# Kernel optimization log

Measured on AMD Instinct MI355X. Metric: run time of the kernel, lower is better.

Reference implementation:

```python
import jax, jax.numpy as jnp
import numpy as np

D = 768          # hidden_size
N_HEADS = 12
HEAD_DIM = D // N_HEADS  # 64
WINDOW = 128 // 2        # local_attention // 2 = 64 tokens each side
ROPE_THETA = 10000.0     # local_rope_theta


def _rope_freqs(T, dtype=jnp.float32):
    # complex rotation factors e^{i * pos * inv_freq}, shape [T, HEAD_DIM//2]
    inv_freq = 1.0 / (ROPE_THETA ** (jnp.arange(0, HEAD_DIM, 2, dtype=dtype) / HEAD_DIM))
    ang = jnp.arange(T, dtype=dtype)[:, None] * inv_freq[None, :]
    return jnp.exp(1j * ang.astype(jnp.complex64))


def _apply_rope(x, freqs):
    # x: [B, T, N, H]; split into (2, H//2) pairs as in the source reshape
    B, T, N, H = x.shape
    pairs = x.reshape(B, T, N, 2, H // 2)
    c = pairs[..., 0, :] + 1j * pairs[..., 1, :]          # [B,T,N,H//2]
    rot = c * freqs[None, :, None, :]                      # broadcast over B, heads
    out = jnp.stack([jnp.real(rot), jnp.imag(rot)], axis=-1)  # [B,T,N,H//2,2]
    return out.reshape(B, T, N, H)  # attention_scaling = 1.0 for default rope


def setup_inputs() -> dict:
    key = jax.random.key(0)
    k1, k2, k3 = jax.random.split(key, 3)
    B, T = 4, 2048
    hidden_states = jax.random.normal(k1, (B, T, D), dtype=jnp.float32)
    attention_mask = jnp.ones((B, T), dtype=jnp.int32)
    Wqkv = jax.random.normal(k2, (3 * D, D), dtype=jnp.float32) * (1.0 / np.sqrt(D))
    Wo = jax.random.normal(k3, (D, D), dtype=jnp.float32) * (1.0 / np.sqrt(D))
    return {"hidden_states": hidden_states, "attention_mask": attention_mask,
            "Wqkv": Wqkv, "Wo": Wo}


def reference(hidden_states, attention_mask, Wqkv, Wo):
    B, T, _ = hidden_states.shape
    # fused QKV projection (no bias in ModernBERT)
    qkv = jnp.einsum('btd,ed->bte', hidden_states, Wqkv)   # [B,T,3D]
    q, k, v = jnp.split(qkv, 3, axis=-1)
    to_heads = lambda x: x.reshape(B, T, N_HEADS, HEAD_DIM)
    q, k, v = to_heads(q), to_heads(k), to_heads(v)
    # rotary embedding (complex multiply)
    freqs = _rope_freqs(T)
    q = _apply_rope(q, freqs)
    k = _apply_rope(k, freqs)
    # sliding-window + padding mask
    pos = jnp.arange(T)
    window = jnp.abs(pos[:, None] - pos[None, :]) <= WINDOW   # [T,T]
    pad = attention_mask.astype(jnp.bool_)                    # [B,T]
    allowed = window[None, None, :, :] & pad[:, None, :, None] & pad[:, None, None, :]
    # eager SDPA
    scale = 1.0 / np.sqrt(HEAD_DIM)
    scores = jnp.einsum('bqnh,bknh->bnqk', q, k) * scale      # [B,N,T,T]
    scores = jnp.where(allowed, scores, jnp.finfo(scores.dtype).min)
    probs = jax.nn.softmax(scores, axis=-1)
    attn = jnp.einsum('bnqk,bknh->bqnh', probs, v)            # [B,T,N,H]
    attn = attn.reshape(B, T, D)
    return jnp.einsum('btd,ed->bte', attn, Wo)                # output proj
```

## Files before the change

### kernel.cpp

```cpp
#include <hip/hip_runtime.h>
#include <hip/hip_bf16.h>
#include <math.h>

#define BATCH 4
#define SEQ   2048
#define DMODEL 768
#define NHEADS 12
#define HDIM  64
#define WIN   64
#define QKV_LD 2304

typedef __attribute__((ext_vector_type(8))) short bf16x8;
typedef __attribute__((ext_vector_type(4))) float f32x4;

typedef __attribute__((address_space(1))) const unsigned int guint;
typedef __attribute__((address_space(3))) unsigned int luint;

__device__ inline void gl_lds16(const __hip_bfloat16* g, __hip_bfloat16* l) {
    __builtin_amdgcn_global_load_lds((guint*)g, (luint*)l, 16, 0, 0);
}

__device__ inline void to_out(float* p, float v) { *p = v; }
__device__ inline void to_out(__hip_bfloat16* p, float v) { *p = __float2bfloat16(v); }

#define N4_HID  (BATCH * SEQ * DMODEL / 4)
#define N4_WQKV (QKV_LD * DMODEL / 4)
#define N4_WO   (DMODEL * DMODEL / 4)
#define N_ROPE  (SEQ * 32)
#define SETUP_TOTAL (N4_HID + N4_WQKV + N4_WO + N_ROPE)

__device__ inline void cast4(const float* in, __hip_bfloat16* out, int i) {
    float4 v = ((const float4*)in)[i];
    union { ushort4 u; __hip_bfloat16 h[4]; } o;
    o.h[0] = __float2bfloat16(v.x); o.h[1] = __float2bfloat16(v.y);
    o.h[2] = __float2bfloat16(v.z); o.h[3] = __float2bfloat16(v.w);
    ((ushort4*)out)[i] = o.u;
}

__global__ __launch_bounds__(256) void setup_kernel(const float* __restrict__ hidden,
                                                    const float* __restrict__ Wqkv,
                                                    const float* __restrict__ Wo,
                                                    __hip_bfloat16* __restrict__ hid_bf,
                                                    __hip_bfloat16* __restrict__ wqkv_bf,
                                                    __hip_bfloat16* __restrict__ wo_bf,
                                                    float2* __restrict__ tab) {
    int id = blockIdx.x * 256 + threadIdx.x;
    if (id < N4_HID) {
        cast4(hidden, hid_bf, id);
    } else if (id < N4_HID + N4_WQKV) {
        cast4(Wqkv, wqkv_bf, id - N4_HID);
    } else if (id < N4_HID + N4_WQKV + N4_WO) {
        cast4(Wo, wo_bf, id - N4_HID - N4_WQKV);
    } else if (id < SETUP_TOTAL) {
        int idx = id - (N4_HID + N4_WQKV + N4_WO);
        int t = idx >> 5, j = idx & 31;
        const float L2T_OVER_32 = 13.287712379549449f / 32.0f;
        float inv = exp2f(-(float)j * L2T_OVER_32);
        float s, c;
        sincosf((float)t * inv, &s, &c);
        tab[idx] = make_float2(c, s);
    }
}

template <typename OutT>
__global__ __launch_bounds__(256) void gemm_nt_bf16(const __hip_bfloat16* __restrict__ A,
                                                    const __hip_bfloat16* __restrict__ B,
                                                    OutT* __restrict__ C,
                                                    int lda, int ldb, int ldc, int K,
                                                    const float2* __restrict__ rope_tab) {
    __shared__ __align__(16) char smem[32768];
    __hip_bfloat16* As = (__hip_bfloat16*)smem;
    __hip_bfloat16* Bs = (__hip_bfloat16*)(smem + 16384);

    const int tid  = threadIdx.x;
    const int lane = tid & 63;
    const int wave = tid >> 6;
    const int wr   = wave >> 1;
    const int wc   = wave & 1;
    const int fr   = lane & 15;
    const int quad = lane >> 4;

    const int bid = blockIdx.x;
    const int x   = bid & 7;
    const int j   = bid >> 3;
    const int m0  = (x * 8 + (j & 7)) * 128;
    const int n0  = (j >> 3) * 128;

    f32x4 acc[4][4];
#pragma unroll
    for (int i = 0; i < 4; i++)
#pragma unroll
        for (int jj = 0; jj < 4; jj++) acc[i][jj] = (f32x4){0.f, 0.f, 0.f, 0.f};

    for (int k0 = 0; k0 < K; k0 += 64) {
        __syncthreads();
#pragma unroll
        for (int c = 0; c < 4; c++) {
            int t = (wave * 4 + c) * 64 + lane;
            int row = t >> 3, ch = t & 7;
            int gcol = (ch ^ (row & 7)) * 8;
            gl_lds16(A + (size_t)(m0 + row) * lda + k0 + gcol, As + t * 8);
            gl_lds16(B + (size_t)(n0 + row) * ldb + k0 + gcol, Bs + t * 8);
        }
        __syncthreads();

#pragma unroll
        for (int ks = 0; ks < 2; ks++) {
            bf16x8 af[4], bf_[4];
#pragma unroll
            for (int mi = 0; mi < 4; mi++) {
                int row = wr * 64 + mi * 16 + fr;
                int pos = (ks * 4 + quad) ^ (row & 7);
                af[mi] = *(const bf16x8*)(As + row * 64 + pos * 8);
            }
#pragma unroll
            for (int ni = 0; ni < 4; ni++) {
                int row = wc * 64 + ni * 16 + fr;
                int pos = (ks * 4 + quad) ^ (row & 7);
                bf_[ni] = *(const bf16x8*)(Bs + row * 64 + pos * 8);
            }
#pragma unroll
            for (int mi = 0; mi < 4; mi++)
#pragma unroll
                for (int ni = 0; ni < 4; ni++)
                    acc[mi][ni] = __builtin_amdgcn_mfma_f32_16x16x32_bf16(af[mi], bf_[ni], acc[mi][ni], 0, 0, 0);
        }
    }

    const int b0 = n0 + wc * 64;
    if (rope_tab != nullptr && b0 < 2 * DMODEL) {
#pragma unroll
        for (int mi = 0; mi < 4; mi++) {
#pragma unroll
            for (int r = 0; r < 4; r++) {
                int t = (m0 + wr * 64 + mi * 16 + quad * 4 + r) & (SEQ - 1);
#pragma unroll
                for (int ni = 0; ni < 2; ni++) {
                    float2 cs = rope_tab[t * 32 + ni * 16 + fr];
                    float x0 = acc[mi][ni][r], x1 = acc[mi][ni + 2][r];
                    acc[mi][ni][r]     = x0 * cs.x - x1 * cs.y;
                    acc[mi][ni + 2][r] = x0 * cs.y + x1 * cs.x;
                }
            }
        }
    }

    __syncthreads();
    OutT* patch = (OutT*)smem + wave * (16 * 72);
    constexpr int NV = sizeof(OutT);

#pragma unroll
    for (int mi = 0; mi < 4; mi++) {
#pragma unroll
        for (int ni = 0; ni < 4; ni++)
#pragma unroll
            for (int r = 0; r < 4; r++)
                to_out(&patch[(quad * 4 + r) * 72 + ni * 16 + fr], acc[mi][ni][r]);
        __syncthreads();
        {
            int prow = lane >> 2, seg = lane & 3;
            const uint4* src = (const uint4*)(patch + prow * 72 + seg * 16);
            OutT* dst = &C[(size_t)(m0 + wr * 64 + mi * 16 + prow) * ldc + b0 + seg * 16];
#pragma unroll
            for (int v = 0; v < NV; v++)
                ((uint4*)dst)[v] = src[v];
        }
        __syncthreads();
    }
}

#define PLD  192

__global__ __launch_bounds__(256) void attn_kernel(const __hip_bfloat16* __restrict__ qkv,
                                                   const int* __restrict__ mask,
                                                   __hip_bfloat16* __restrict__ attn) {
    __shared__ __align__(16) char smem[49152];
    __hip_bfloat16* Ks = (__hip_bfloat16*)smem;
    __hip_bfloat16* Pb = (__hip_bfloat16*)smem;
    __hip_bfloat16* Vt = (__hip_bfloat16*)(smem + 24576);

    const int tid  = threadIdx.x;
    const int lane = tid & 63;
    const int wave = tid >> 6;
    const int fr   = lane & 15;
    const int quad = lane >> 4;

    const int bid  = blockIdx.x;
    const int x    = bid & 7;
    const int j    = bid >> 3;
    const int b    = x >> 1;
    const int q0   = ((x & 1) * 16 + (j & 15)) * 64;
    const int head = j >> 4;

    const int klo = max(0, q0 - WIN);
    const int khi = min(SEQ, q0 + 64 + WIN);
    const int nk  = khi - klo;
    const int nt  = nk >> 4;
    const int nkc = nk >> 5;

    const size_t rowbase = (size_t)(b * SEQ) * QKV_LD + head * HDIM;

    for (int task = tid; task < nk * 8; task += 256) {
        int row = task >> 3, g = task & 7;
        uint4 v = *(const uint4*)(qkv + rowbase + (size_t)(klo + row) * QKV_LD + DMODEL + g * 8);
        *(uint4*)(Ks + row * 64 + (g ^ (row & 7)) * 8) = v;
    }
    {
        int h = lane;
        const __hip_bfloat16* vb = qkv + rowbase + 2 * DMODEL + h;
        int ng = nk >> 3;
        for (int g = wave; g < ng; g += 4) {
            unsigned int u0, u1, u2, u3;
            {
                unsigned short a0 = *(const unsigned short*)(vb + (size_t)(klo + g * 8 + 0) * QKV_LD);
                unsigned short a1 = *(const unsigned short*)(vb + (size_t)(klo + g * 8 + 1) * QKV_LD);
                unsigned short a2 = *(const unsigned short*)(vb + (size_t)(klo + g * 8 + 2) * QKV_LD);
                unsigned short a3 = *(const unsigned short*)(vb + (size_t)(klo + g * 8 + 3) * QKV_LD);
                unsigned short a4 = *(const unsigned short*)(vb + (size_t)(klo + g * 8 + 4) * QKV_LD);
                unsigned short a5 = *(const unsigned short*)(vb + (size_t)(klo + g * 8 + 5) * QKV_LD);
                unsigned short a6 = *(const unsigned short*)(vb + (size_t)(klo + g * 8 + 6) * QKV_LD);
                unsigned short a7 = *(const unsigned short*)(vb + (size_t)(klo + g * 8 + 7) * QKV_LD);
                u0 = (unsigned int)a0 | ((unsigned int)a1 << 16);
                u1 = (unsigned int)a2 | ((unsigned int)a3 << 16);
                u2 = (unsigned int)a4 | ((unsigned int)a5 << 16);
                u3 = (unsigned int)a6 | ((unsigned int)a7 << 16);
            }
            int cs = g ^ (h & 7);
            *(uint4*)(Vt + h * PLD + cs * 8) = make_uint4(u0, u1, u2, u3);
        }
    }

    const int qrow0 = q0 + wave * 16;
    bf16x8 aq0 = *(const bf16x8*)(qkv + rowbase + (size_t)(qrow0 + fr) * QKV_LD + quad * 8);
    bf16x8 aq1 = *(const bf16x8*)(qkv + rowbase + (size_t)(qrow0 + fr) * QKV_LD + 32 + quad * 8);

    const int* mb = mask + b * SEQ;
    int mq[4];
#pragma unroll
    for (int r = 0; r < 4; r++) mq[r] = mb[qrow0 + quad * 4 + r];

    __syncthreads();

    f32x4 sc[12];
#pragma unroll
    for (int kt = 0; kt < 12; kt++) sc[kt] = (f32x4){-1e30f, -1e30f, -1e30f, -1e30f};

#pragma unroll
    for (int kt = 0; kt < 12; kt++) {
        if (kt < nt) {
            int krow = kt * 16 + fr;
            int kg = klo + krow;
            int p0 = (quad) ^ (krow & 7);
            int p1 = (4 + quad) ^ (krow & 7);
            bf16x8 bk0 = *(const bf16x8*)(Ks + krow * 64 + p0 * 8);
            bf16x8 bk1 = *(const bf16x8*)(Ks + krow * 64 + p1 * 8);
            f32x4 a = (f32x4){0.f, 0.f, 0.f, 0.f};
            a = __builtin_amdgcn_mfma_f32_16x16x32_bf16(aq0, bk0, a, 0, 0, 0);
            a = __builtin_amdgcn_mfma_f32_16x16x32_bf16(aq1, bk1, a, 0, 0, 0);
            int mk = mb[kg];
            f32x4 s;
#pragma unroll
            for (int r = 0; r < 4; r++) {
                int qg = qrow0 + quad * 4 + r;
                bool ok = (abs(qg - kg) <= WIN) && (mk != 0) && (mq[r] != 0);
                s[r] = ok ? a[r] * 0.125f : -1e30f;
            }
            sc[kt] = s;
        }
    }

    f32x4 mx = sc[0];
#pragma unroll
    for (int kt = 1; kt < 12; kt++)
#pragma unroll
        for (int r = 0; r < 4; r++) mx[r] = fmaxf(mx[r], sc[kt][r]);
#pragma unroll
    for (int off = 8; off >= 1; off >>= 1)
#pragma unroll
        for (int r = 0; r < 4; r++) mx[r] = fmaxf(mx[r], __shfl_xor(mx[r], off));

    f32x4 sum = (f32x4){0.f, 0.f, 0.f, 0.f};
#pragma unroll
    for (int kt = 0; kt < 12; kt++)
#pragma unroll
        for (int r = 0; r < 4; r++) {
            float e = __expf(sc[kt][r] - mx[r]);
            sc[kt][r] = e;
            sum[r] += e;
        }
#pragma unroll
    for (int off = 8; off >= 1; off >>= 1)
#pragma unroll
        for (int r = 0; r < 4; r++) sum[r] += __shfl_xor(sum[r], off);
    f32x4 rs;
#pragma unroll
    for (int r = 0; r < 4; r++) rs[r] = 1.0f / sum[r];

    __syncthreads();
#pragma unroll
    for (int kt = 0; kt < 12; kt++) {
        if (kt < nt) {
#pragma unroll
            for (int r = 0; r < 4; r++) {
                int prow = wave * 16 + quad * 4 + r;
                int c = kt * 2 + (fr >> 3);
                int cs = c ^ (prow & 7);
                Pb[prow * PLD + cs * 8 + (fr & 7)] = __float2bfloat16(sc[kt][r] * rs[r]);
            }
        }
    }
    __syncthreads();

    f32x4 o[4];
#pragma unroll
    for (int ht = 0; ht < 4; ht++) o[ht] = (f32x4){0.f, 0.f, 0.f, 0.f};

#pragma unroll
    for (int kc = 0; kc < 6; kc++) {
        if (kc < nkc) {
            int cs = (kc * 4 + quad) ^ (fr & 7);
            bf16x8 ap = *(const bf16x8*)(Pb + (wave * 16 + fr) * PLD + cs * 8);
#pragma unroll
            for (int ht = 0; ht < 4; ht++) {
                bf16x8 bv = *(const bf16x8*)(Vt + (ht * 16 + fr) * PLD + cs * 8);
                o[ht] = __builtin_amdgcn_mfma_f32_16x16x32_bf16(ap, bv, o[ht], 0, 0, 0);
            }
        }
    }

    __hip_bfloat16* ob = attn + (size_t)(b * SEQ + qrow0) * DMODEL + head * HDIM;
#pragma unroll
    for (int r = 0; r < 4; r++)
#pragma unroll
        for (int ht = 0; ht < 4; ht++)
            ob[(size_t)(quad * 4 + r) * DMODEL + ht * 16 + fr] = __float2bfloat16(o[ht][r]);
}

extern "C" void kernel_launch(void* const* d_in, const int* in_sizes, int n_in,
                              void* d_out, int out_size, void* d_ws, size_t ws_size,
                              hipStream_t stream) {
    const float* hidden = (const float*)d_in[0];
    const int*   mask   = (const int*)d_in[1];
    const float* Wqkv   = (const float*)d_in[2];
    const float* Wo     = (const float*)d_in[3];
    float* out = (float*)d_out;

    char* w = (char*)d_ws;
    __hip_bfloat16* qkv_bf  = (__hip_bfloat16*)(w);
    __hip_bfloat16* hid_bf  = (__hip_bfloat16*)(w + 37748736);
    __hip_bfloat16* wqkv_bf = (__hip_bfloat16*)(w + 50331648);
    __hip_bfloat16* wo_bf   = (__hip_bfloat16*)(w + 53870592);
    __hip_bfloat16* attn_bf = (__hip_bfloat16*)(w + 55050240);
    float2*         tab     = (float2*)(w + 67633152);

    setup_kernel<<<SETUP_TOTAL / 256, 256, 0, stream>>>(hidden, Wqkv, Wo,
                                                        hid_bf, wqkv_bf, wo_bf, tab);

    gemm_nt_bf16<__hip_bfloat16><<<18 * 64, 256, 0, stream>>>(hid_bf, wqkv_bf, qkv_bf,
                                                              DMODEL, DMODEL, QKV_LD, DMODEL, tab);

    attn_kernel<<<(SEQ / 64) * NHEADS * BATCH, 256, 0, stream>>>(qkv_bf, mask, attn_bf);

    gemm_nt_bf16<float><<<6 * 64, 256, 0, stream>>>(attn_bf, wo_bf, out,
                                                    DMODEL, DMODEL, DMODEL, DMODEL, nullptr);
}
```

Measured before the change: 192.1 us.

## Template GEMM tile width, use 128x64 tiles for output projection, direct stores

The GEMM kernel gains an NWN template parameter controlling the N tile width. The output projection now uses 128x64 tiles, giving 768 blocks instead of 384, to fill more CUs on the small GEMM. The QKV GEMM keeps 128x128 tiles. The LDS-staged coalesced epilogue is replaced by direct per-element global stores, which removes barriers and LDS traffic but produces strided, poorly coalesced writes.

```diff
diff --git a/kernel.cpp b/kernel.cpp
--- a/kernel.cpp
+++ b/kernel.cpp
@@ -62,21 +62,25 @@
     }
 }
 
-template <typename OutT>
+template <typename OutT, int NWN>
 __global__ __launch_bounds__(256) void gemm_nt_bf16(const __hip_bfloat16* __restrict__ A,
                                                     const __hip_bfloat16* __restrict__ B,
                                                     OutT* __restrict__ C,
                                                     int lda, int ldb, int ldc, int K,
                                                     const float2* __restrict__ rope_tab) {
-    __shared__ __align__(16) char smem[32768];
-    __hip_bfloat16* As = (__hip_bfloat16*)smem;
-    __hip_bfloat16* Bs = (__hip_bfloat16*)(smem + 16384);
+    constexpr int BN  = 64 * NWN;
+    constexpr int NWM = 4 / NWN;
+    constexpr int WM  = 128 / NWM;
+    constexpr int MI  = WM / 16;
+
+    __shared__ __align__(16) __hip_bfloat16 As[128 * 64];
+    __shared__ __align__(16) __hip_bfloat16 Bs[BN * 64];
 
     const int tid  = threadIdx.x;
     const int lane = tid & 63;
     const int wave = tid >> 6;
-    const int wr   = wave >> 1;
-    const int wc   = wave & 1;
+    const int wm   = wave / NWN;
+    const int wn   = wave % NWN;
     const int fr   = lane & 15;
     const int quad = lane >> 4;
 
@@ -84,11 +88,11 @@
     const int x   = bid & 7;
     const int j   = bid >> 3;
     const int m0  = (x * 8 + (j & 7)) * 128;
-    const int n0  = (j >> 3) * 128;
-
-    f32x4 acc[4][4];
-#pragma unroll
-    for (int i = 0; i < 4; i++)
+    const int n0  = (j >> 3) * BN;
+
+    f32x4 acc[MI][4];
+#pragma unroll
+    for (int i = 0; i < MI; i++)
 #pragma unroll
         for (int jj = 0; jj < 4; jj++) acc[i][jj] = (f32x4){0.f, 0.f, 0.f, 0.f};
 
@@ -100,40 +104,46 @@
             int row = t >> 3, ch = t & 7;
             int gcol = (ch ^ (row & 7)) * 8;
             gl_lds16(A + (size_t)(m0 + row) * lda + k0 + gcol, As + t * 8);
+        }
+#pragma unroll
+        for (int c = 0; c < 2 * NWN; c++) {
+            int t = (wave * 2 * NWN + c) * 64 + lane;
+            int row = t >> 3, ch = t & 7;
+            int gcol = (ch ^ (row & 7)) * 8;
             gl_lds16(B + (size_t)(n0 + row) * ldb + k0 + gcol, Bs + t * 8);
         }
         __syncthreads();
 
 #pragma unroll
         for (int ks = 0; ks < 2; ks++) {
-            bf16x8 af[4], bf_[4];
-#pragma unroll
-            for (int mi = 0; mi < 4; mi++) {
-                int row = wr * 64 + mi * 16 + fr;
+            bf16x8 af[MI], bf_[4];
+#pragma unroll
+            for (int mi = 0; mi < MI; mi++) {
+                int row = wm * WM + mi * 16 + fr;
                 int pos = (ks * 4 + quad) ^ (row & 7);
                 af[mi] = *(const bf16x8*)(As + row * 64 + pos * 8);
             }
 #pragma unroll
             for (int ni = 0; ni < 4; ni++) {
-                int row = wc * 64 + ni * 16 + fr;
+                int row = wn * 64 + ni * 16 + fr;
                 int pos = (ks * 4 + quad) ^ (row & 7);
                 bf_[ni] = *(const bf16x8*)(Bs + row * 64 + pos * 8);
             }
 #pragma unroll
-            for (int mi = 0; mi < 4; mi++)
+            for (int mi = 0; mi < MI; mi++)
 #pragma unroll
                 for (int ni = 0; ni < 4; ni++)
                     acc[mi][ni] = __builtin_amdgcn_mfma_f32_16x16x32_bf16(af[mi], bf_[ni], acc[mi][ni], 0, 0, 0);
         }
     }
 
-    const int b0 = n0 + wc * 64;
+    const int b0 = n0 + wn * 64;
     if (rope_tab != nullptr && b0 < 2 * DMODEL) {
 #pragma unroll
-        for (int mi = 0; mi < 4; mi++) {
+        for (int mi = 0; mi < MI; mi++) {
 #pragma unroll
             for (int r = 0; r < 4; r++) {
-                int t = (m0 + wr * 64 + mi * 16 + quad * 4 + r) & (SEQ - 1);
+                int t = (m0 + wm * WM + mi * 16 + quad * 4 + r) & (SEQ - 1);
 #pragma unroll
                 for (int ni = 0; ni < 2; ni++) {
                     float2 cs = rope_tab[t * 32 + ni * 16 + fr];
@@ -145,28 +155,17 @@
         }
     }
 
-    __syncthreads();
-    OutT* patch = (OutT*)smem + wave * (16 * 72);
-    constexpr int NV = sizeof(OutT);
-
-#pragma unroll
-    for (int mi = 0; mi < 4; mi++) {
-#pragma unroll
-        for (int ni = 0; ni < 4; ni++)
+#pragma unroll
+    for (int mi = 0; mi < MI; mi++)
+#pragma unroll
+        for (int ni = 0; ni < 4; ni++) {
+            f32x4 v = acc[mi][ni];
+            int gc = b0 + ni * 16 + fr;
+            size_t rbase = (size_t)(m0 + wm * WM + mi * 16 + quad * 4);
 #pragma unroll
             for (int r = 0; r < 4; r++)
-                to_out(&patch[(quad * 4 + r) * 72 + ni * 16 + fr], acc[mi][ni][r]);
-        __syncthreads();
-        {
-            int prow = lane >> 2, seg = lane & 3;
-            const uint4* src = (const uint4*)(patch + prow * 72 + seg * 16);
-            OutT* dst = &C[(size_t)(m0 + wr * 64 + mi * 16 + prow) * ldc + b0 + seg * 16];
-#pragma unroll
-            for (int v = 0; v < NV; v++)
-                ((uint4*)dst)[v] = src[v];
-        }
-        __syncthreads();
-    }
+                to_out(&C[(rbase + r) * ldc + gc], v[r]);
+        }
 }
 
 #define PLD  192
@@ -356,11 +355,11 @@
     setup_kernel<<<SETUP_TOTAL / 256, 256, 0, stream>>>(hidden, Wqkv, Wo,
                                                         hid_bf, wqkv_bf, wo_bf, tab);
 
-    gemm_nt_bf16<__hip_bfloat16><<<18 * 64, 256, 0, stream>>>(hid_bf, wqkv_bf, qkv_bf,
-                                                              DMODEL, DMODEL, QKV_LD, DMODEL, tab);
+    gemm_nt_bf16<__hip_bfloat16, 2><<<18 * 64, 256, 0, stream>>>(hid_bf, wqkv_bf, qkv_bf,
+                                                                 DMODEL, DMODEL, QKV_LD, DMODEL, tab);
 
     attn_kernel<<<(SEQ / 64) * NHEADS * BATCH, 256, 0, stream>>>(qkv_bf, mask, attn_bf);
 
-    gemm_nt_bf16<float><<<6 * 64, 256, 0, stream>>>(attn_bf, wo_bf, out,
-                                                    DMODEL, DMODEL, DMODEL, DMODEL, nullptr);
-}
+    gemm_nt_bf16<float, 1><<<12 * 64, 256, 0, stream>>>(attn_bf, wo_bf, out,
+                                                        DMODEL, DMODEL, DMODEL, DMODEL, nullptr);
+}
```

Measured after the change: 182.3 us. -5.1%, faster.
